# Performance work log

Hardware: AMD Instinct MI355X
Metric: run time of the kernel (lower is better)

Reference implementation:

```python
import jax, jax.numpy as jnp
import numpy as np

B, T, H, O = 128, 512, 1024, 128


def setup_inputs() -> dict:
    key = jax.random.key(0)
    ks = jax.random.split(key, 9)
    s = 0.05  # small init scale for numerical sanity
    return {
        "y_hist": jax.random.normal(ks[0], (B, T), jnp.float32),
        "W_ih": jax.random.normal(ks[1], (4 * H, 1), jnp.float32) * s,
        "W_hh": jax.random.normal(ks[2], (4 * H, H), jnp.float32) * s,
        "b_ih": jax.random.normal(ks[3], (4 * H,), jnp.float32) * s,
        "b_hh": jax.random.normal(ks[4], (4 * H,), jnp.float32) * s,
        "fc_W": jax.random.normal(ks[5], (O, H), jnp.float32) * s,
        "fc_b": jax.random.normal(ks[6], (O,), jnp.float32) * s,
        # stands in for the xavier-initialized (1,B,H) h0/c0 of the original
        "h0": jax.random.normal(ks[7], (B, H), jnp.float32) * s,
        "c0": jax.random.normal(ks[8], (B, H), jnp.float32) * s,
    }


def reference(y_hist, W_ih, W_hh, b_ih, b_hh, fc_W, fc_b, h0, c0):
    # PyTorch LSTM cell, gate order (i, f, g, o); input feature size is 1.
    Hs = W_hh.shape[1]
    w_ih = W_ih[:, 0]          # (4H,)
    b = b_ih + b_hh            # (4H,)

    def step(carry, x_t):
        h, c = carry           # (B,H), (B,H)
        gates = h @ W_hh.T + x_t[:, None] * w_ih + b  # (B,4H)
        i, f, g, o = jnp.split(gates, 4, axis=-1)
        c = jax.nn.sigmoid(f) * c + jax.nn.sigmoid(i) * jnp.tanh(g)
        h = jax.nn.sigmoid(o) * jnp.tanh(c)
        return (h, c), None

    (h_T, _), _ = jax.lax.scan(step, (h0, c0), y_hist.T)  # scan over time (T,B)
    return h_T @ fc_W.T + fc_b  # (B, O)
```

## Files before the change

kernel.cpp:

```cpp
#include <hip/hip_runtime.h>
#include <hip/hip_fp16.h>

typedef _Float16 half8 __attribute__((ext_vector_type(8)));
typedef float f32x4 __attribute__((ext_vector_type(4)));

#define T_STEPS 512

static __device__ __forceinline__ float sigf(float x) {
    return __builtin_amdgcn_rcpf(1.0f + __builtin_amdgcn_exp2f(-1.44269504088896f * x));
}
static __device__ __forceinline__ float tanhf_fast(float x) {
    return 2.0f * __builtin_amdgcn_rcpf(1.0f + __builtin_amdgcn_exp2f(-2.88539008177793f * x)) - 1.0f;
}

__global__ __launch_bounds__(512, 2) void lstm_persist(
    const float* __restrict__ y_hist,
    const float* __restrict__ W_ih,
    const float* __restrict__ W_hh,
    const float* __restrict__ b_ih,
    const float* __restrict__ b_hh,
    const float* __restrict__ fc_W,
    const float* __restrict__ fc_b,
    const float* __restrict__ h0,
    const float* __restrict__ c0,
    float* __restrict__ out,
    unsigned long long* __restrict__ hbuf0,
    unsigned long long* __restrict__ hbuf1,
    float* __restrict__ hfin,
    unsigned int* __restrict__ flags,
    unsigned int* __restrict__ xcnt,
    unsigned int* __restrict__ gbar)
{
    __shared__ _Float16 h_lds[16 * 1024];
    __shared__ float    y_lds[512][16];
    __shared__ unsigned long long hout_lds[128];
    __shared__ unsigned sjj[2];

    const int tid = threadIdx.x;
    const int l   = tid & 63;
    const int wid = tid >> 6;
    const int q4  = l >> 4;
    const int n   = l & 15;

    if (tid == 0) {
        unsigned x;
        asm volatile("s_getreg_b32 %0, hwreg(HW_REG_XCC_ID)" : "=s"(x));
        x &= 7u;
        sjj[0] = x;
        sjj[1] = atomicAdd(&xcnt[x], 1u) & 31u;
    }
    __syncthreads();
    const int s  = (int)sjj[0];
    const int jj = (int)sjj[1];

    if (jj == 0 && tid < 32)
        *(volatile unsigned*)&flags[((s << 5) + tid) << 5] = 0u;
    asm volatile("s_waitcnt vmcnt(0)" ::: "memory");
    __syncthreads();
    if (tid == 0) {
        __hip_atomic_fetch_add(&gbar[s], 1u, __ATOMIC_RELAXED, __HIP_MEMORY_SCOPE_AGENT);
        int guard = 0;
        while (__hip_atomic_load(&gbar[s], __ATOMIC_RELAXED, __HIP_MEMORY_SCOPE_AGENT) < 32u) {
            if (++guard > (1 << 20)) break;
        }
    }
    __syncthreads();

    half8 wfrag[32];
    {
        const int r16  = l & 15;
        const int u_a  = 4 * wid + (r16 >> 2);
        const int g_a  = r16 & 3;
        const int grow = g_a * 1024 + 32 * jj + u_a;
        const float* wrow = W_hh + (size_t)grow * 1024 + 8 * q4;
        #pragma unroll
        for (int c = 0; c < 32; ++c) {
            f32x4 a0 = *(const f32x4*)(wrow + 32 * c);
            f32x4 a1 = *(const f32x4*)(wrow + 32 * c + 4);
            half8 w;
            w[0]=(_Float16)a0[0]; w[1]=(_Float16)a0[1];
            w[2]=(_Float16)a0[2]; w[3]=(_Float16)a0[3];
            w[4]=(_Float16)a1[0]; w[5]=(_Float16)a1[1];
            w[6]=(_Float16)a1[2]; w[7]=(_Float16)a1[3];
            wfrag[c] = w;
        }
    }

    const int u_e = 4 * wid + q4;
    float wih_r[4], bias_r[4], creg;
    #pragma unroll
    for (int g = 0; g < 4; ++g) {
        const int gr = g * 1024 + 32 * jj + u_e;
        wih_r[g]  = W_ih[gr];
        bias_r[g] = b_ih[gr] + b_hh[gr];
    }
    creg = c0[(size_t)(16 * s + n) * 1024 + 32 * jj + u_e];

    {
        const int r = tid >> 5, sg = tid & 31;
        const float* yr = y_hist + (size_t)(16 * s + r) * 512;
        #pragma unroll
        for (int e = 0; e < 4; ++e) {
            f32x4 v = *(const f32x4*)(yr + sg * 4 + 128 * e);
            #pragma unroll
            for (int j = 0; j < 4; ++j) y_lds[sg * 4 + 128 * e + j][r] = v[j];
        }
    }
    {
        const int r = tid >> 5, sg = tid & 31;
        const int swz0 = (r & 7) << 4;
        const float* hr = h0 + (size_t)(16 * s + r) * 1024 + sg * 32;
        char* db = (char*)h_lds + r * 2048;
        #pragma unroll
        for (int v = 0; v < 4; ++v) {
            f32x4 a0 = *(const f32x4*)(hr + 8 * v);
            f32x4 a1 = *(const f32x4*)(hr + 8 * v + 4);
            half8 hv;
            hv[0]=(_Float16)a0[0]; hv[1]=(_Float16)a0[1];
            hv[2]=(_Float16)a0[2]; hv[3]=(_Float16)a0[3];
            hv[4]=(_Float16)a1[0]; hv[5]=(_Float16)a1[1];
            hv[6]=(_Float16)a1[2]; hv[7]=(_Float16)a1[3];
            *(half8*)(db + ((sg * 64 + 16 * v) ^ swz0)) = hv;
        }
    }
    __syncthreads();

    const int bb  = n * 2048 + 16 * q4;
    const int swz = (n & 7) << 4;
    const volatile unsigned* fpoll = flags + (((s << 5) + (l & 31)) << 5);

    for (int t = 0; t < T_STEPS; ++t) {
        if (t > 0) {
            if (wid == 0) {
                int guard = 0;
                for (;;) {
                    unsigned fv = *fpoll;
                    if (__all((int)(fv >= (unsigned)t))) break;
                    if (++guard > (1 << 15)) break;
                    __builtin_amdgcn_fence(__ATOMIC_ACQUIRE, "agent");
                }
                __builtin_amdgcn_fence(__ATOMIC_ACQUIRE, "agent");
            }
            __syncthreads();
            const unsigned long long* gb = ((t & 1) ? hbuf1 : hbuf0) + (s << 12);
            #pragma unroll
            for (int i = 0; i < 8; ++i) {
                const int F = ((i * 512 + tid) + (jj << 9)) & 4095;
                unsigned long long v = gb[F];
                const int n2 = (F >> 3) & 15;
                const int off = ((n2 * 2048) + ((F >> 7) << 6) + ((F & 7) << 3))
                                ^ ((n2 & 7) << 4);
                *(unsigned long long*)((char*)h_lds + off) = v;
            }
            __syncthreads();
        }

        f32x4 ac0 = {0.f,0.f,0.f,0.f}, ac1 = {0.f,0.f,0.f,0.f};
        f32x4 ac2 = {0.f,0.f,0.f,0.f}, ac3 = {0.f,0.f,0.f,0.f};
        {
            const char* hb = (const char*)h_lds;
            #pragma unroll
            for (int c = 0; c < 8; ++c) {
                half8 b0 = *(const half8*)(hb + ((bb + 64 * c) ^ swz));
                half8 b1 = *(const half8*)(hb + ((bb + 64 * (c + 8)) ^ swz));
                half8 b2 = *(const half8*)(hb + ((bb + 1024 + 64 * c) ^ swz));
                half8 b3 = *(const half8*)(hb + ((bb + 1024 + 64 * (c + 8)) ^ swz));
                ac0 = __builtin_amdgcn_mfma_f32_16x16x32_f16(wfrag[c],      b0, ac0, 0, 0, 0);
                ac1 = __builtin_amdgcn_mfma_f32_16x16x32_f16(wfrag[c + 8],  b1, ac1, 0, 0, 0);
                ac2 = __builtin_amdgcn_mfma_f32_16x16x32_f16(wfrag[c + 16], b2, ac2, 0, 0, 0);
                ac3 = __builtin_amdgcn_mfma_f32_16x16x32_f16(wfrag[c + 24], b3, ac3, 0, 0, 0);
            }
        }
        {
            const float yt = y_lds[t][n];
            float gi = (ac0[0] + ac1[0]) + (ac2[0] + ac3[0]) + yt * wih_r[0] + bias_r[0];
            float gf = (ac0[1] + ac1[1]) + (ac2[1] + ac3[1]) + yt * wih_r[1] + bias_r[1];
            float gg = (ac0[2] + ac1[2]) + (ac2[2] + ac3[2]) + yt * wih_r[2] + bias_r[2];
            float go = (ac0[3] + ac1[3]) + (ac2[3] + ac3[3]) + yt * wih_r[3] + bias_r[3];
            float cn = sigf(gf) * creg + sigf(gi) * tanhf_fast(gg);
            creg = cn;
            float hv = sigf(go) * tanhf_fast(cn);
            ((_Float16*)hout_lds)[n * 32 + u_e] = (_Float16)hv;
            if (t == T_STEPS - 1) {
                hfin[(size_t)(16 * s + n) * 1024 + 32 * jj + u_e] = hv;
                asm volatile("s_waitcnt vmcnt(0)" ::: "memory");
            }
        }
        __syncthreads();
        if (wid == 0) {
            unsigned long long* ob = ((t & 1) ? hbuf0 : hbuf1) + (s << 12) + (jj << 7);
            ob[l]      = hout_lds[l];
            ob[l + 64] = hout_lds[l + 64];
            asm volatile("s_waitcnt vmcnt(0)" ::: "memory");
            if (l == 0)
                *(volatile unsigned*)&flags[((s << 5) + jj) << 5] = (unsigned)(t + 1);
        }
    }

    if (jj < 16) {
        if (wid == 0) {
            int guard = 0;
            for (;;) {
                unsigned fv = *fpoll;
                if (__all((int)(fv >= (unsigned)T_STEPS))) break;
                if (++guard > (1 << 15)) break;
                __builtin_amdgcn_fence(__ATOMIC_ACQUIRE, "agent");
            }
            __builtin_amdgcn_fence(__ATOMIC_ACQUIRE, "agent");
        }
        __syncthreads();
        __builtin_amdgcn_fence(__ATOMIC_ACQUIRE, "agent");
        float* hT  = (float*)h_lds;
        float* red = hT + 1024;
        const int b = 16 * s + jj;
        if (tid < 256) {
            f32x4 v = *(const f32x4*)(hfin + (size_t)b * 1024 + tid * 4);
            *(f32x4*)(hT + tid * 4) = v;
        }
        __syncthreads();
        {
            const int o = tid & 127, kq = tid >> 7;
            const float* wr = fc_W + (size_t)o * 1024 + kq * 256;
            const float* hp = hT + kq * 256;
            float p = 0.0f;
            #pragma unroll 8
            for (int i = 0; i < 256; i += 4) {
                f32x4 a = *(const f32x4*)(hp + i);
                f32x4 w = *(const f32x4*)(wr + i);
                p += a[0]*w[0] + a[1]*w[1] + a[2]*w[2] + a[3]*w[3];
            }
            red[kq * 128 + o] = p;
        }
        __syncthreads();
        if (tid < 128) {
            out[(size_t)b * 128 + tid] =
                red[tid] + red[128 + tid] + red[256 + tid] + red[384 + tid] + fc_b[tid];
        }
    }
}

extern "C" void kernel_launch(void* const* d_in, const int* in_sizes, int n_in,
                              void* d_out, int out_size, void* d_ws, size_t ws_size,
                              hipStream_t stream) {
    (void)in_sizes; (void)n_in; (void)out_size; (void)ws_size;
    const float* y_hist = (const float*)d_in[0];
    const float* W_ih   = (const float*)d_in[1];
    const float* W_hh   = (const float*)d_in[2];
    const float* b_ih   = (const float*)d_in[3];
    const float* b_hh   = (const float*)d_in[4];
    const float* fc_W   = (const float*)d_in[5];
    const float* fc_b   = (const float*)d_in[6];
    const float* h0     = (const float*)d_in[7];
    const float* c0     = (const float*)d_in[8];

    char* ws = (char*)d_ws;
    unsigned long long* hbuf0 = (unsigned long long*)ws;
    unsigned long long* hbuf1 = (unsigned long long*)(ws + (256 << 10));
    float*    hfin  = (float*)(ws + (512 << 10));
    unsigned int* flags = (unsigned int*)(ws + (1024 << 10));
    unsigned int* xcnt  = (unsigned int*)(ws + (1024 << 10) + (32 << 10));
    unsigned int* gbar  = (unsigned int*)(ws + (1024 << 10) + (32 << 10) + 128);

    hipMemsetAsync(ws + (1024 << 10) + (32 << 10), 0, 1024, stream);
    hipLaunchKernelGGL(lstm_persist, dim3(256), dim3(512), 16384, stream,
                       y_hist, W_ih, W_hh, b_ih, b_hh, fc_W, fc_b, h0, c0,
                       (float*)d_out, hbuf0, hbuf1, hfin, flags, xcnt, gbar);
}
```

Before: 2.306 ms.

## Replace flag-based step barrier with step-tagged hidden-state words polled directly

Each hidden value is packed with its step number into a 32-bit word and written straight to global memory. Consumers poll the data itself until every tag matches, which removes the separate flag write, the vmcnt waits, the LDS staging of outputs, and the startup grid barrier. The LDS h buffer is double-buffered so each step needs only one __syncthreads. The cost is double-size global traffic per step, plus reliance on word-level store visibility ordering without an explicit release fence. The hfin buffer is dropped because the final h is read from the tagged buffer.

```diff
diff --git a/kernel.cpp b/kernel.cpp
--- a/kernel.cpp
+++ b/kernel.cpp
@@ -3,6 +3,9 @@
 
 typedef _Float16 half8 __attribute__((ext_vector_type(8)));
 typedef float f32x4 __attribute__((ext_vector_type(4)));
+typedef unsigned int uint4v __attribute__((ext_vector_type(4)));
+typedef unsigned int u32;
+typedef unsigned long long u64;
 
 #define T_STEPS 512
 
@@ -24,16 +27,12 @@
     const float* __restrict__ h0,
     const float* __restrict__ c0,
     float* __restrict__ out,
-    unsigned long long* __restrict__ hbuf0,
-    unsigned long long* __restrict__ hbuf1,
-    float* __restrict__ hfin,
-    unsigned int* __restrict__ flags,
-    unsigned int* __restrict__ xcnt,
-    unsigned int* __restrict__ gbar)
+    u32* __restrict__ hbuf0,
+    u32* __restrict__ hbuf1,
+    u32* __restrict__ xcnt)
 {
-    __shared__ _Float16 h_lds[16 * 1024];
+    __shared__ _Float16 h_lds[2][16 * 1024];
     __shared__ float    y_lds[512][16];
-    __shared__ unsigned long long hout_lds[128];
     __shared__ unsigned sjj[2];
 
     const int tid = threadIdx.x;
@@ -52,19 +51,6 @@
     __syncthreads();
     const int s  = (int)sjj[0];
     const int jj = (int)sjj[1];
-
-    if (jj == 0 && tid < 32)
-        *(volatile unsigned*)&flags[((s << 5) + tid) << 5] = 0u;
-    asm volatile("s_waitcnt vmcnt(0)" ::: "memory");
-    __syncthreads();
-    if (tid == 0) {
-        __hip_atomic_fetch_add(&gbar[s], 1u, __ATOMIC_RELAXED, __HIP_MEMORY_SCOPE_AGENT);
-        int guard = 0;
-        while (__hip_atomic_load(&gbar[s], __ATOMIC_RELAXED, __HIP_MEMORY_SCOPE_AGENT) < 32u) {
-            if (++guard > (1 << 20)) break;
-        }
-    }
-    __syncthreads();
 
     half8 wfrag[32];
     {
@@ -110,7 +96,7 @@
         const int r = tid >> 5, sg = tid & 31;
         const int swz0 = (r & 7) << 4;
         const float* hr = h0 + (size_t)(16 * s + r) * 1024 + sg * 32;
-        char* db = (char*)h_lds + r * 2048;
+        char* db = (char*)(&h_lds[0][0]) + r * 2048;
         #pragma unroll
         for (int v = 0; v < 4; ++v) {
             f32x4 a0 = *(const f32x4*)(hr + 8 * v);
@@ -123,42 +109,57 @@
             *(half8*)(db + ((sg * 64 + 16 * v) ^ swz0)) = hv;
         }
     }
-    __syncthreads();
 
     const int bb  = n * 2048 + 16 * q4;
     const int swz = (n & 7) << 4;
-    const volatile unsigned* fpoll = flags + (((s << 5) + (l & 31)) << 5);
 
     for (int t = 0; t < T_STEPS; ++t) {
         if (t > 0) {
-            if (wid == 0) {
-                int guard = 0;
-                for (;;) {
-                    unsigned fv = *fpoll;
-                    if (__all((int)(fv >= (unsigned)t))) break;
-                    if (++guard > (1 << 15)) break;
-                    __builtin_amdgcn_fence(__ATOMIC_ACQUIRE, "agent");
+            const uint4v* gq = (const uint4v*)(((t & 1) ? hbuf1 : hbuf0) + (s << 14));
+            const u32 tgt = (u32)t;
+            int F[8];
+            uint4v v[8];
+            #pragma unroll
+            for (int i = 0; i < 8; ++i)
+                F[i] = ((i * 512 + tid) + (jj << 7)) & 4095;
+            unsigned ok = 0;
+            int rounds = 0;
+            __builtin_amdgcn_fence(__ATOMIC_ACQUIRE, "agent");
+            for (;;) {
+                #pragma unroll
+                for (int i = 0; i < 8; ++i) {
+                    if (!((ok >> i) & 1u)) {
+                        uint4v x = gq[F[i]];
+                        v[i] = x;
+                        bool f = ((x.x >> 16) == tgt) & ((x.y >> 16) == tgt) &
+                                 ((x.z >> 16) == tgt) & ((x.w >> 16) == tgt);
+                        ok |= (unsigned)f << i;
+                    }
                 }
+                if (__all((int)(ok == 0xffu))) break;
+                if (++rounds > (1 << 13)) break;
                 __builtin_amdgcn_fence(__ATOMIC_ACQUIRE, "agent");
             }
-            __syncthreads();
-            const unsigned long long* gb = ((t & 1) ? hbuf1 : hbuf0) + (s << 12);
+            char* hb = (char*)(&h_lds[t & 1][0]);
             #pragma unroll
             for (int i = 0; i < 8; ++i) {
-                const int F = ((i * 512 + tid) + (jj << 9)) & 4095;
-                unsigned long long v = gb[F];
-                const int n2 = (F >> 3) & 15;
-                const int off = ((n2 * 2048) + ((F >> 7) << 6) + ((F & 7) << 3))
-                                ^ ((n2 & 7) << 4);
-                *(unsigned long long*)((char*)h_lds + off) = v;
-            }
-            __syncthreads();
-        }
+                const int Fi = F[i];
+                const int n2 = (Fi >> 3) & 15;
+                int off = (n2 * 2048) + ((Fi >> 7) << 6) + ((Fi & 7) << 3);
+                off ^= (n2 & 7) << 4;
+                u64 d = (u64)(v[i].x & 0xffffu)
+                      | ((u64)(v[i].y & 0xffffu) << 16)
+                      | ((u64)(v[i].z & 0xffffu) << 32)
+                      | ((u64)(v[i].w & 0xffffu) << 48);
+                *(u64*)(hb + off) = d;
+            }
+        }
+        __syncthreads();
 
         f32x4 ac0 = {0.f,0.f,0.f,0.f}, ac1 = {0.f,0.f,0.f,0.f};
         f32x4 ac2 = {0.f,0.f,0.f,0.f}, ac3 = {0.f,0.f,0.f,0.f};
         {
-            const char* hb = (const char*)h_lds;
+            const char* hb = (const char*)(&h_lds[t & 1][0]);
             #pragma unroll
             for (int c = 0; c < 8; ++c) {
                 half8 b0 = *(const half8*)(hb + ((bb + 64 * c) ^ swz));
@@ -180,42 +181,41 @@
             float cn = sigf(gf) * creg + sigf(gi) * tanhf_fast(gg);
             creg = cn;
             float hv = sigf(go) * tanhf_fast(cn);
-            ((_Float16*)hout_lds)[n * 32 + u_e] = (_Float16)hv;
-            if (t == T_STEPS - 1) {
-                hfin[(size_t)(16 * s + n) * 1024 + 32 * jj + u_e] = hv;
-                asm volatile("s_waitcnt vmcnt(0)" ::: "memory");
-            }
-        }
-        __syncthreads();
-        if (wid == 0) {
-            unsigned long long* ob = ((t & 1) ? hbuf0 : hbuf1) + (s << 12) + (jj << 7);
-            ob[l]      = hout_lds[l];
-            ob[l + 64] = hout_lds[l + 64];
-            asm volatile("s_waitcnt vmcnt(0)" ::: "memory");
-            if (l == 0)
-                *(volatile unsigned*)&flags[((s << 5) + jj) << 5] = (unsigned)(t + 1);
+            const unsigned short hu =
+                __builtin_bit_cast(unsigned short, (_Float16)hv);
+            const u32 pv = ((u32)(t + 1) << 16) | (u32)hu;
+            u32* ob = ((((t + 1) & 1) ? hbuf1 : hbuf0))
+                      + (s << 14) + (jj << 9) + (n << 5) + u_e;
+            *ob = pv;
         }
     }
 
     if (jj < 16) {
-        if (wid == 0) {
-            int guard = 0;
+        float* hT  = (float*)y_lds;
+        float* red = hT + 1024;
+        if (tid < 256) {
+            const int jjp = tid >> 3, u8 = tid & 7;
+            const uint4v* gq = (const uint4v*)(hbuf0 + (s << 14));
+            const int idx = jjp * 128 + jj * 8 + u8;
+            uint4v x;
+            int rounds = 0;
+            __builtin_amdgcn_fence(__ATOMIC_ACQUIRE, "agent");
             for (;;) {
-                unsigned fv = *fpoll;
-                if (__all((int)(fv >= (unsigned)T_STEPS))) break;
-                if (++guard > (1 << 15)) break;
+                x = gq[idx];
+                bool f = ((x.x >> 16) == (u32)T_STEPS) & ((x.y >> 16) == (u32)T_STEPS) &
+                         ((x.z >> 16) == (u32)T_STEPS) & ((x.w >> 16) == (u32)T_STEPS);
+                if (__all((int)f)) break;
+                if (++rounds > (1 << 14)) break;
                 __builtin_amdgcn_fence(__ATOMIC_ACQUIRE, "agent");
             }
-            __builtin_amdgcn_fence(__ATOMIC_ACQUIRE, "agent");
-        }
-        __syncthreads();
-        __builtin_amdgcn_fence(__ATOMIC_ACQUIRE, "agent");
-        float* hT  = (float*)h_lds;
-        float* red = hT + 1024;
-        const int b = 16 * s + jj;
-        if (tid < 256) {
-            f32x4 v = *(const f32x4*)(hfin + (size_t)b * 1024 + tid * 4);
-            *(f32x4*)(hT + tid * 4) = v;
+            hT[jjp * 32 + u8 * 4 + 0] =
+                (float)__builtin_bit_cast(_Float16, (unsigned short)(x.x & 0xffffu));
+            hT[jjp * 32 + u8 * 4 + 1] =
+                (float)__builtin_bit_cast(_Float16, (unsigned short)(x.y & 0xffffu));
+            hT[jjp * 32 + u8 * 4 + 2] =
+                (float)__builtin_bit_cast(_Float16, (unsigned short)(x.z & 0xffffu));
+            hT[jjp * 32 + u8 * 4 + 3] =
+                (float)__builtin_bit_cast(_Float16, (unsigned short)(x.w & 0xffffu));
         }
         __syncthreads();
         {
@@ -233,7 +233,7 @@
         }
         __syncthreads();
         if (tid < 128) {
-            out[(size_t)b * 128 + tid] =
+            out[(size_t)(16 * s + jj) * 128 + tid] =
                 red[tid] + red[128 + tid] + red[256 + tid] + red[384 + tid] + fc_b[tid];
         }
     }
@@ -254,15 +254,12 @@
     const float* c0     = (const float*)d_in[8];
 
     char* ws = (char*)d_ws;
-    unsigned long long* hbuf0 = (unsigned long long*)ws;
-    unsigned long long* hbuf1 = (unsigned long long*)(ws + (256 << 10));
-    float*    hfin  = (float*)(ws + (512 << 10));
-    unsigned int* flags = (unsigned int*)(ws + (1024 << 10));
-    unsigned int* xcnt  = (unsigned int*)(ws + (1024 << 10) + (32 << 10));
-    unsigned int* gbar  = (unsigned int*)(ws + (1024 << 10) + (32 << 10) + 128);
-
-    hipMemsetAsync(ws + (1024 << 10) + (32 << 10), 0, 1024, stream);
-    hipLaunchKernelGGL(lstm_persist, dim3(256), dim3(512), 16384, stream,
+    u32* hbuf0 = (u32*)ws;
+    u32* hbuf1 = (u32*)(ws + (512 << 10));
+    u32* xcnt  = (u32*)(ws + (1024 << 10));
+
+    hipMemsetAsync(xcnt, 0, 128, stream);
+    hipLaunchKernelGGL(lstm_persist, dim3(256), dim3(512), 0, stream,
                        y_hist, W_ih, W_hh, b_ih, b_hh, fc_W, fc_b, h0, c0,
-                       (float*)d_out, hbuf0, hbuf1, hfin, flags, xcnt, gbar);
-}
+                       (float*)d_out, hbuf0, hbuf1, xcnt);
+}
```

Result: slower. 8.588 ms (+272.5%).
